# Optimization experiments

Measured on AMD Instinct MI355X. Metric: run time of the kernel, lower is better.

The kernel has to match this reference:

```python
import jax, jax.numpy as jnp
import numpy as np

LEAK = 0.01  # nn.LeakyReLU default slope


def _guide(x, w1, w3, b3, bias):
    # x: [N, 3, H, W]
    c_in = x.shape[1]
    x1 = jax.nn.leaky_relu(jnp.einsum('oi,nihw->nohw', w1[:, :, 0, 0], x), LEAK)
    x3 = jax.lax.conv_general_dilated(x, w3, (1, 1), 'SAME') + b3[None, :, None, None]
    x3 = jax.nn.leaky_relu(x3, LEAK)
    g = jnp.sum(x1 + x3, axis=1, keepdims=True) / c_in + bias[0]
    return jnp.clip(g, 0.0, 1.0)  # [N, 1, H, W]


def _slice(grid, guide):
    # grid: [N, C=12, D=12, GH=16, GW=16]; guide: [N, 1, H, W] in [0, 1]
    # Trilinear, align_corners=True grid_sample semantics.
    N, C, D, GH, GW = grid.shape
    H, W = guide.shape[2], guide.shape[3]
    fy = (jnp.arange(H, dtype=grid.dtype) / (H - 1)) * (GH - 1)   # [H]
    fx = (jnp.arange(W, dtype=grid.dtype) / (W - 1)) * (GW - 1)   # [W]
    fz = guide[:, 0] * (D - 1)                                    # [N, H, W]
    y0 = jnp.floor(fy).astype(jnp.int32); ty = fy - y0
    x0 = jnp.floor(fx).astype(jnp.int32); tx = fx - x0
    z0 = jnp.floor(fz).astype(jnp.int32); tz = fz - z0

    def slice_one(g, z0b, tzb):
        # g: [C, D, GH, GW]; z0b, tzb: [H, W]
        out = jnp.zeros((C, H, W), g.dtype)
        for dz in (0, 1):
            wz = (1.0 - tzb) if dz == 0 else tzb              # [H, W]
            zi = jnp.clip(z0b + dz, 0, D - 1)                 # [H, W]
            for dy in (0, 1):
                wy = (1.0 - ty) if dy == 0 else ty            # [H]
                yi = jnp.clip(y0 + dy, 0, GH - 1)             # [H]
                for dx in (0, 1):
                    wx = (1.0 - tx) if dx == 0 else tx        # [W]
                    xi = jnp.clip(x0 + dx, 0, GW - 1)         # [W]
                    corner = g[:, zi, yi[:, None], xi[None, :]]   # [C, H, W]
                    out = out + corner * (wz * wy[:, None] * wx[None, :])[None]
        return out

    return jax.vmap(slice_one)(grid, z0, tz)  # [N, 12, H, W]


def _apply(coeff, full):
    # coeff: [N, 12, H, W] -> 3x4 per-pixel affine on RGB
    N, _, H, W = coeff.shape
    c = coeff.reshape(N, 3, 4, H, W)
    return jnp.einsum('ncihw,nihw->nchw', c[:, :, :3], full) + c[:, :, 3]


def setup_inputs() -> dict:
    key = jax.random.key(0)
    ks = jax.random.split(key, 5)
    N, H, W = 4, 1024, 1024
    grid = jax.random.normal(ks[0], (N, 12, 12, 16, 16), jnp.float32)
    fullres = jax.random.uniform(ks[1], (N, 3, H, W), jnp.float32)
    # Guide conv1x1 initialized as identity + tiny noise (as in original)
    w1 = (jnp.eye(3, dtype=jnp.float32)
          + jax.random.normal(ks[2], (1,), jnp.float32)[0] * 1e-4).reshape(3, 3, 1, 1)
    w3 = jax.random.normal(ks[3], (3, 3, 3, 3), jnp.float32) * 0.1
    b3 = jax.random.normal(ks[4], (3,), jnp.float32) * 0.1
    guide_bias = jnp.zeros((1,), jnp.float32)
    return {"grid": grid, "fullres": fullres, "w1": w1, "w3": w3,
            "b3": b3, "guide_bias": guide_bias}


def reference(grid, fullres, w1, w3, b3, guide_bias):
    guide = _guide(fullres, w1, w3, b3, guide_bias)
    sliced = _slice(grid, guide)
    return _apply(sliced, fullres)
```

## Files before the change

### kernel.cpp

```cpp
#include <hip/hip_runtime.h>

#define LEAK 0.01f

typedef float v2f __attribute__((ext_vector_type(2)));
typedef _Float16 h2 __attribute__((ext_vector_type(2)));

constexpr int H = 1024, W = 1024, NIMG = 4;
constexpr int GC = 12, GD = 12, GH = 16, GW = 16;
constexpr int NZ = GD - 1;
constexpr int CELLE = NZ * GC;
constexpr int CF4 = 33;

constexpr int PX = 4;
constexpr int BX = 64, BY = 4;
constexpr int TILE_W = BX * PX;
constexpr int XS = 6;

constexpr int IMROWS = BY + 2;
constexpr int IMW    = 268;
constexpr int IMC4   = IMW / 4;
constexpr int IMCH   = IMROWS * IMW;

static __device__ __forceinline__ h2 bch2(float f) {
    return __builtin_bit_cast(h2, f);
}
static __device__ __forceinline__ float bcf(h2 v) {
    return __builtin_bit_cast(float, v);
}
static __device__ __forceinline__ h2 pkrtz(float a, float b) {
    return __builtin_bit_cast(h2, __builtin_amdgcn_cvt_pkrtz(a, b));
}

static __device__ __forceinline__ float fdot2f(h2 a, h2 b, float c) {
#if __has_builtin(__builtin_amdgcn_fdot2)
    return __builtin_amdgcn_fdot2(a, b, c, false);
#else
    return (float)a.x * (float)b.x + (float)a.y * (float)b.y + c;
#endif
}

__global__ __launch_bounds__(256) void pairgen(const float* __restrict__ grid,
                                               h2* __restrict__ table) {
    const int n  = blockIdx.x / NZ;
    const int z0 = blockIdx.x % NZ;
    const int yx = threadIdx.x;
    const float* src = grid + (size_t)n * GC * GD * GH * GW + yx;
    h2* dst = table + ((size_t)n * 256 + yx) * CELLE + z0 * GC;
    #pragma unroll
    for (int c = 0; c < GC; ++c) {
        float a = src[(c * GD + z0) * 256];
        float b = src[(c * GD + z0 + 1) * 256];
        dst[c] = pkrtz(a, b);
    }
}

__global__ __launch_bounds__(256) void hdrnet_fused(
    const float* __restrict__ grid,
    const float* __restrict__ full,
    const float* __restrict__ w1,
    const float* __restrict__ w3,
    const float* __restrict__ b3,
    const float* __restrict__ bias,
    const h2* __restrict__ table,
    float* __restrict__ out)
{
    __shared__ __align__(16) float simg[3 * IMCH];
    __shared__ __align__(16) h2 sgrid[BY * XS * CELLE];

    const int n  = blockIdx.z;
    const int wb = blockIdx.x * TILE_W;
    const int hb = blockIdx.y * BY;

    const float scale = 15.0f / 1023.0f;
    const int xlo = (int)(wb * scale);

    const int tid = threadIdx.y * BX + threadIdx.x;
    const size_t plane = (size_t)H * W;
    const float* fn = full + (size_t)n * 3 * plane;

    for (int e = tid; e < 3 * IMROWS * IMC4; e += BX * BY) {
        int ch = e / (IMROWS * IMC4);
        int t  = e - ch * (IMROWS * IMC4);
        int r  = t / IMC4, m = t - r * IMC4;
        int yy = hb + r - 1;
        int gx = wb - 4 + 4 * m;
        float4 v = (float4){0.0f, 0.0f, 0.0f, 0.0f};
        if ((unsigned)yy < (unsigned)H && (unsigned)gx < (unsigned)W)
            v = *(const float4*)(fn + (size_t)ch * plane + (size_t)yy * W + gx);
        *(float4*)&simg[ch * IMCH + r * IMW + 4 * m] = v;
    }

    if (table) {
        const float4* tsrc = (const float4*)(table + (size_t)n * 256 * CELLE);
        float4* sdst = (float4*)sgrid;
        for (int e = tid; e < BY * XS * CF4; e += BX * BY) {
            int r  = e / (XS * CF4);
            int t  = e - r * (XS * CF4);
            int lx = t / CF4, q = t - lx * CF4;
            int yy = hb + r;
            float fy = (float)yy * scale;
            int y0 = min((int)fy, GH - 2);
            float ty = fy - (float)y0;
            _Float16 t1 = (_Float16)ty, t0 = (_Float16)(1.0f - ty);
            h2 w0v = (h2){t0, t0}, w1v = (h2){t1, t1};
            int xi = min(xlo + lx, GW - 1);
            const float4* pa = tsrc + (y0 * GW + xi) * CF4 + q;
            const float4* pb = tsrc + ((y0 + 1) * GW + xi) * CF4 + q;
            float4 A = *pa, B = *pb, R;
            R.x = bcf(bch2(A.x) * w0v + bch2(B.x) * w1v);
            R.y = bcf(bch2(A.y) * w0v + bch2(B.y) * w1v);
            R.z = bcf(bch2(A.z) * w0v + bch2(B.z) * w1v);
            R.w = bcf(bch2(A.w) * w0v + bch2(B.w) * w1v);
            sdst[e] = R;
        }
    } else {
        const float* gnn = grid + (size_t)n * GC * GD * GH * GW;
        for (int e = tid; e < BY * XS * CELLE; e += BX * BY) {
            int r  = e / (XS * CELLE);
            int t  = e - r * (XS * CELLE);
            int lx = t / CELLE, u = t - lx * CELLE;
            int z0 = u / GC, c = u - z0 * GC;
            int yy = hb + r;
            float fy = (float)yy * scale;
            int y0 = min((int)fy, GH - 2);
            float ty = fy - (float)y0;
            int xi = min(xlo + lx, GW - 1);
            const float* gp = gnn + ((c * GD + z0) * GH + y0) * GW + xi;
            float a0 = gp[0],  a1 = gp[256];
            float b0 = gp[16], b1 = gp[272];
            sgrid[e] = pkrtz(fmaf(b0 - a0, ty, a0), fmaf(b1 - a1, ty, a1));
        }
    }
    __syncthreads();

    const int h  = hb + threadIdx.y;
    const int w0 = wb + threadIdx.x * PX;

    float w1c[3][3];
    #pragma unroll
    for (int o = 0; o < 3; ++o)
        #pragma unroll
        for (int i = 0; i < 3; ++i)
            w1c[o][i] = w1[o * 3 + i];
    const float biasv = bias[0];

    v2f a3p[3][2];
    #pragma unroll
    for (int o = 0; o < 3; ++o) {
        float b = b3[o];
        a3p[o][0] = (v2f){b, b};
        a3p[o][1] = (v2f){b, b};
    }
    float rgb[3][PX];

    #pragma unroll
    for (int i = 0; i < 3; ++i) {
        #pragma unroll
        for (int dy = 0; dy < 3; ++dy) {
            const float* rowp = &simg[i * IMCH + (threadIdx.y + dy) * IMW
                                      + (threadIdx.x << 2)];
            float  lhalo = rowp[3];
            float4 a = *(const float4*)(rowp + 4);
            float4 b4 = *(const float4*)(rowp + 8);
            float row[8];
            row[0] = lhalo;
            row[1] = a.x;  row[2] = a.y;  row[3] = a.z;  row[4] = a.w;
            row[5] = b4.x; row[6] = b4.y; row[7] = b4.z;
            if (dy == 1) {
                #pragma unroll
                for (int j = 0; j < PX; ++j) rgb[i][j] = row[1 + j];
            }
            #pragma unroll
            for (int o = 0; o < 3; ++o) {
                const float* kp = w3 + ((o * 3 + i) * 3 + dy) * 3;
                #pragma unroll
                for (int t = 0; t < 3; ++t) {
                    const float kt = kp[t];
                    v2f kv = (v2f){kt, kt};
                    a3p[o][0] = __builtin_elementwise_fma(
                        kv, (v2f){row[t], row[t + 1]}, a3p[o][0]);
                    a3p[o][1] = __builtin_elementwise_fma(
                        kv, (v2f){row[t + 2], row[t + 3]}, a3p[o][1]);
                }
            }
        }
    }

    const int srow = threadIdx.y * XS;
    const float4* sg4 = (const float4*)sgrid;

    float4 ov0, ov1, ov2;
    float* ov0p = &ov0.x; float* ov1p = &ov1.x; float* ov2p = &ov2.x;

    #pragma unroll
    for (int j = 0; j < PX; ++j) {
        float gacc = 0.0f;
        #pragma unroll
        for (int o = 0; o < 3; ++o) {
            float x1 = fmaf(w1c[o][0], rgb[0][j],
                       fmaf(w1c[o][1], rgb[1][j], w1c[o][2] * rgb[2][j]));
            x1 = (x1 > 0.0f) ? x1 : LEAK * x1;
            float x3 = a3p[o][j >> 1][j & 1];
            x3 = (x3 > 0.0f) ? x3 : LEAK * x3;
            gacc += x1 + x3;
        }
        float g = fmaf(gacc, (1.0f / 3.0f), biasv);
        g = fminf(fmaxf(g, 0.0f), 1.0f);

        float fx = (float)(w0 + j) * scale;
        int x0 = (int)fx;
        x0 = min(x0, GW - 2);
        float tx = fx - (float)x0;
        const int lxr = x0 - xlo;

        float fz = g * 11.0f;
        int z0 = (int)fz;
        z0 = min(z0, GD - 2);
        float tz = fz - (float)z0;
        h2 hz = pkrtz(1.0f - tz, tz);
        _Float16 hx0 = (_Float16)(1.0f - tx), hx1 = (_Float16)tx;
        h2 wA = hz * (h2){hx0, hx0};
        h2 wB = hz * (h2){hx1, hx1};

        const float4* pA = sg4 + (srow + lxr) * CF4 + z0 * 3;
        const float4* pB = pA + CF4;
        float4 A0 = pA[0], A1 = pA[1], A2 = pA[2];
        float4 B0 = pB[0], B1 = pB[1], B2 = pB[2];

        float co[12];
        co[0]  = fdot2f(wA, bch2(A0.x), fdot2f(wB, bch2(B0.x), 0.0f));
        co[1]  = fdot2f(wA, bch2(A0.y), fdot2f(wB, bch2(B0.y), 0.0f));
        co[2]  = fdot2f(wA, bch2(A0.z), fdot2f(wB, bch2(B0.z), 0.0f));
        co[3]  = fdot2f(wA, bch2(A0.w), fdot2f(wB, bch2(B0.w), 0.0f));
        co[4]  = fdot2f(wA, bch2(A1.x), fdot2f(wB, bch2(B1.x), 0.0f));
        co[5]  = fdot2f(wA, bch2(A1.y), fdot2f(wB, bch2(B1.y), 0.0f));
        co[6]  = fdot2f(wA, bch2(A1.z), fdot2f(wB, bch2(B1.z), 0.0f));
        co[7]  = fdot2f(wA, bch2(A1.w), fdot2f(wB, bch2(B1.w), 0.0f));
        co[8]  = fdot2f(wA, bch2(A2.x), fdot2f(wB, bch2(B2.x), 0.0f));
        co[9]  = fdot2f(wA, bch2(A2.y), fdot2f(wB, bch2(B2.y), 0.0f));
        co[10] = fdot2f(wA, bch2(A2.z), fdot2f(wB, bch2(B2.z), 0.0f));
        co[11] = fdot2f(wA, bch2(A2.w), fdot2f(wB, bch2(B2.w), 0.0f));

        const float r = rgb[0][j], gg = rgb[1][j], b = rgb[2][j];
        ov0p[j] = fmaf(co[0], r, fmaf(co[1],  gg, fmaf(co[2],  b, co[3])));
        ov1p[j] = fmaf(co[4], r, fmaf(co[5],  gg, fmaf(co[6],  b, co[7])));
        ov2p[j] = fmaf(co[8], r, fmaf(co[9],  gg, fmaf(co[10], b, co[11])));
    }

    float* ob = out + (size_t)n * 3 * plane + (size_t)h * W + w0;
    *(float4*)(ob)             = ov0;
    *(float4*)(ob + plane)     = ov1;
    *(float4*)(ob + 2 * plane) = ov2;
}

extern "C" void kernel_launch(void* const* d_in, const int* in_sizes, int n_in,
                              void* d_out, int out_size, void* d_ws, size_t ws_size,
                              hipStream_t stream) {
    const float* grid_p = (const float*)d_in[0];
    const float* full_p = (const float*)d_in[1];
    const float* w1_p   = (const float*)d_in[2];
    const float* w3_p   = (const float*)d_in[3];
    const float* b3_p   = (const float*)d_in[4];
    const float* bias_p = (const float*)d_in[5];
    float* out_p = (float*)d_out;

    const size_t tbytes = (size_t)NIMG * 256 * CELLE * sizeof(h2);
    h2* table = (d_ws && ws_size >= tbytes) ? (h2*)d_ws : nullptr;

    if (table) {
        hipLaunchKernelGGL(pairgen, dim3(NIMG * NZ), dim3(256), 0, stream,
                           grid_p, table);
    }

    dim3 block(BX, BY, 1);
    dim3 grid_dim(W / TILE_W, H / BY, NIMG);
    hipLaunchKernelGGL(hdrnet_fused, grid_dim, block, 0, stream,
                       grid_p, full_p, w1_p, w3_p, b3_p, bias_p, table, out_p);
}
```

Measured before the change: 46.29 us.

## Store image tile as fp16 in LDS and prefetch grid table into registers

The shared-memory copy of the full-resolution image tile is now packed to fp16 pairs, which halves its LDS footprint. The grid-table loads are hoisted into registers before the image staging so that their latency overlaps the image loads. The barrier is moved so the 3x3 convolution can run while the bilinear grid blend is being written, and launch bounds now request 6 waves for occupancy. In exchange, the guide input and the pixel RGB values used in the affine transform lose precision through fp16 rounding, and register pressure goes up.

```diff
diff --git a/kernel.cpp b/kernel.cpp
--- a/kernel.cpp
+++ b/kernel.cpp
@@ -15,11 +15,12 @@
 constexpr int BX = 64, BY = 4;
 constexpr int TILE_W = BX * PX;
 constexpr int XS = 6;
+constexpr int SGN = BY * XS * CF4;
 
 constexpr int IMROWS = BY + 2;
-constexpr int IMW    = 268;
-constexpr int IMC4   = IMW / 4;
-constexpr int IMCH   = IMROWS * IMW;
+constexpr int IMW2   = 136;
+constexpr int IMCH2  = IMROWS * IMW2;
+constexpr int IMCHUNK = 67;
 
 static __device__ __forceinline__ h2 bch2(float f) {
     return __builtin_bit_cast(h2, f);
@@ -54,7 +55,7 @@
     }
 }
 
-__global__ __launch_bounds__(256) void hdrnet_fused(
+__global__ __launch_bounds__(256, 6) void hdrnet_fused(
     const float* __restrict__ grid,
     const float* __restrict__ full,
     const float* __restrict__ w1,
@@ -64,7 +65,7 @@
     const h2* __restrict__ table,
     float* __restrict__ out)
 {
-    __shared__ __align__(16) float simg[3 * IMCH];
+    __shared__ __align__(16) h2 simgh[3 * IMCH2];
     __shared__ __align__(16) h2 sgrid[BY * XS * CELLE];
 
     const int n  = blockIdx.z;
@@ -78,35 +79,59 @@
     const size_t plane = (size_t)H * W;
     const float* fn = full + (size_t)n * 3 * plane;
 
-    for (int e = tid; e < 3 * IMROWS * IMC4; e += BX * BY) {
-        int ch = e / (IMROWS * IMC4);
-        int t  = e - ch * (IMROWS * IMC4);
-        int r  = t / IMC4, m = t - r * IMC4;
+    float4 tA[4], tB[4];
+    const bool ttail = (tid < SGN - 768);
+    if (table) {
+        const float4* tsrc = (const float4*)(table + (size_t)n * 256 * CELLE);
+        #pragma unroll
+        for (int it = 0; it < 3; ++it) {
+            int e  = tid + 256 * it;
+            int r  = e / (XS * CF4);
+            int t2 = e - r * (XS * CF4);
+            int lx = t2 / CF4, q = t2 - lx * CF4;
+            int y0 = min((int)((float)(hb + r) * scale), GH - 2);
+            int xi = min(xlo + lx, GW - 1);
+            tA[it] = tsrc[(y0 * GW + xi) * CF4 + q];
+            tB[it] = tsrc[((y0 + 1) * GW + xi) * CF4 + q];
+        }
+        if (ttail) {
+            int e  = 768 + tid;
+            int r  = e / (XS * CF4);
+            int t2 = e - r * (XS * CF4);
+            int lx = t2 / CF4, q = t2 - lx * CF4;
+            int y0 = min((int)((float)(hb + r) * scale), GH - 2);
+            int xi = min(xlo + lx, GW - 1);
+            tA[3] = tsrc[(y0 * GW + xi) * CF4 + q];
+            tB[3] = tsrc[((y0 + 1) * GW + xi) * CF4 + q];
+        }
+    }
+
+    for (int e = tid; e < 3 * IMROWS * IMCHUNK; e += BX * BY) {
+        int ch = e / (IMROWS * IMCHUNK);
+        int t  = e - ch * (IMROWS * IMCHUNK);
+        int r  = t / IMCHUNK, m = t - r * IMCHUNK;
         int yy = hb + r - 1;
-        int gx = wb - 4 + 4 * m;
+        int gx = wb - 8 + 4 * m;
         float4 v = (float4){0.0f, 0.0f, 0.0f, 0.0f};
         if ((unsigned)yy < (unsigned)H && (unsigned)gx < (unsigned)W)
             v = *(const float4*)(fn + (size_t)ch * plane + (size_t)yy * W + gx);
-        *(float4*)&simg[ch * IMCH + r * IMW + 4 * m] = v;
-    }
+        *(float2*)&simgh[(ch * IMROWS + r) * IMW2 + 2 * m] =
+            (float2){bcf(pkrtz(v.x, v.y)), bcf(pkrtz(v.z, v.w))};
+    }
+    __syncthreads();
 
     if (table) {
-        const float4* tsrc = (const float4*)(table + (size_t)n * 256 * CELLE);
         float4* sdst = (float4*)sgrid;
-        for (int e = tid; e < BY * XS * CF4; e += BX * BY) {
-            int r  = e / (XS * CF4);
-            int t  = e - r * (XS * CF4);
-            int lx = t / CF4, q = t - lx * CF4;
-            int yy = hb + r;
-            float fy = (float)yy * scale;
-            int y0 = min((int)fy, GH - 2);
-            float ty = fy - (float)y0;
+        #pragma unroll
+        for (int it = 0; it < 4; ++it) {
+            if (it == 3 && !ttail) break;
+            int e = (it == 3) ? (768 + tid) : (tid + 256 * it);
+            int r = e / (XS * CF4);
+            float fy = (float)(hb + r) * scale;
+            float ty = fy - (float)min((int)fy, GH - 2);
             _Float16 t1 = (_Float16)ty, t0 = (_Float16)(1.0f - ty);
             h2 w0v = (h2){t0, t0}, w1v = (h2){t1, t1};
-            int xi = min(xlo + lx, GW - 1);
-            const float4* pa = tsrc + (y0 * GW + xi) * CF4 + q;
-            const float4* pb = tsrc + ((y0 + 1) * GW + xi) * CF4 + q;
-            float4 A = *pa, B = *pb, R;
+            float4 A = tA[it], B = tB[it], R;
             R.x = bcf(bch2(A.x) * w0v + bch2(B.x) * w1v);
             R.y = bcf(bch2(A.y) * w0v + bch2(B.y) * w1v);
             R.z = bcf(bch2(A.z) * w0v + bch2(B.z) * w1v);
@@ -120,8 +145,7 @@
             int t  = e - r * (XS * CELLE);
             int lx = t / CELLE, u = t - lx * CELLE;
             int z0 = u / GC, c = u - z0 * GC;
-            int yy = hb + r;
-            float fy = (float)yy * scale;
+            float fy = (float)(hb + r) * scale;
             int y0 = min((int)fy, GH - 2);
             float ty = fy - (float)y0;
             int xi = min(xlo + lx, GW - 1);
@@ -131,7 +155,6 @@
             sgrid[e] = pkrtz(fmaf(b0 - a0, ty, a0), fmaf(b1 - a1, ty, a1));
         }
     }
-    __syncthreads();
 
     const int h  = hb + threadIdx.y;
     const int w0 = wb + threadIdx.x * PX;
@@ -157,15 +180,19 @@
     for (int i = 0; i < 3; ++i) {
         #pragma unroll
         for (int dy = 0; dy < 3; ++dy) {
-            const float* rowp = &simg[i * IMCH + (threadIdx.y + dy) * IMW
-                                      + (threadIdx.x << 2)];
-            float  lhalo = rowp[3];
-            float4 a = *(const float4*)(rowp + 4);
-            float4 b4 = *(const float4*)(rowp + 8);
+            const h2* rowp = &simgh[(i * IMROWS + threadIdx.y + dy) * IMW2
+                                    + 2 * threadIdx.x];
+            h2 hh = rowp[3];
+            float2 m01 = *(const float2*)(rowp + 4);
+            float2 m23 = *(const float2*)(rowp + 6);
+            h2 q0 = bch2(m01.x), q1 = bch2(m01.y);
+            h2 q2 = bch2(m23.x), q3 = bch2(m23.y);
             float row[8];
-            row[0] = lhalo;
-            row[1] = a.x;  row[2] = a.y;  row[3] = a.z;  row[4] = a.w;
-            row[5] = b4.x; row[6] = b4.y; row[7] = b4.z;
+            row[0] = (float)hh.y;
+            row[1] = (float)q0.x; row[2] = (float)q0.y;
+            row[3] = (float)q1.x; row[4] = (float)q1.y;
+            row[5] = (float)q2.x; row[6] = (float)q2.y;
+            row[7] = (float)q3.x;
             if (dy == 1) {
                 #pragma unroll
                 for (int j = 0; j < PX; ++j) rgb[i][j] = row[1 + j];
@@ -185,6 +212,7 @@
             }
         }
     }
+    __syncthreads();
 
     const int srow = threadIdx.y * XS;
     const float4* sg4 = (const float4*)sgrid;
```

Measured after the change: 47.42 us. 2.5% more time.
